# Kernel tuning notes

Hardware: AMD Instinct MI355X
Metric: run time of the kernel (lower is better)

## Reference

```python
import jax, jax.numpy as jnp
import numpy as np

N_NODES = 10000
N_EDGES = 60000
D = 128          # latent_size
L = 15           # num_layers
EPS = 1e-5       # LayerNorm eps (torch default)


def _layernorm(h, g, b):
    mu = jnp.mean(h, axis=-1, keepdims=True)
    var = jnp.mean(jnp.square(h - mu), axis=-1, keepdims=True)
    return (h - mu) * jax.lax.rsqrt(var + EPS) * g + b


def _mlp(h, w1, b1, g1, bt1, w2, b2, g2, bt2):
    # Linear -> LayerNorm -> GELU(exact) -> [Dropout: identity in eval] -> Linear -> LayerNorm
    h = _layernorm(h @ w1 + b1, g1, bt1)
    h = jax.nn.gelu(h, approximate=False)
    return _layernorm(h @ w2 + b2, g2, bt2)


def setup_inputs() -> dict:
    key = jax.random.key(0)
    ks = jax.random.split(key, 20)
    x = jax.random.normal(ks[0], (N_NODES, D), dtype=jnp.float32)
    edge_index = jax.random.randint(ks[1], (2, N_EDGES), 0, N_NODES, dtype=jnp.int32)
    edge_attr = jax.random.normal(ks[2], (N_EDGES, D), dtype=jnp.float32)
    s = 0.02
    # Edge MLP params: Linear(3D->2D), LN(2D), Linear(2D->D), LN(D), stacked over L layers
    ew1 = jax.random.normal(ks[3], (L, 3 * D, 2 * D), dtype=jnp.float32) * s
    eb1 = jnp.zeros((L, 2 * D), dtype=jnp.float32)
    eg1 = jnp.ones((L, 2 * D), dtype=jnp.float32)
    ebt1 = jnp.zeros((L, 2 * D), dtype=jnp.float32)
    ew2 = jax.random.normal(ks[4], (L, 2 * D, D), dtype=jnp.float32) * s
    eb2 = jnp.zeros((L, D), dtype=jnp.float32)
    eg2 = jnp.ones((L, D), dtype=jnp.float32)
    ebt2 = jnp.zeros((L, D), dtype=jnp.float32)
    # Node MLP params: Linear(2D->2D), LN(2D), Linear(2D->D), LN(D)
    nw1 = jax.random.normal(ks[5], (L, 2 * D, 2 * D), dtype=jnp.float32) * s
    nb1 = jnp.zeros((L, 2 * D), dtype=jnp.float32)
    ng1 = jnp.ones((L, 2 * D), dtype=jnp.float32)
    nbt1 = jnp.zeros((L, 2 * D), dtype=jnp.float32)
    nw2 = jax.random.normal(ks[6], (L, 2 * D, D), dtype=jnp.float32) * s
    nb2 = jnp.zeros((L, D), dtype=jnp.float32)
    ng2 = jnp.ones((L, D), dtype=jnp.float32)
    nbt2 = jnp.zeros((L, D), dtype=jnp.float32)
    return dict(x=x, edge_index=edge_index, edge_attr=edge_attr,
                ew1=ew1, eb1=eb1, eg1=eg1, ebt1=ebt1, ew2=ew2, eb2=eb2, eg2=eg2, ebt2=ebt2,
                nw1=nw1, nb1=nb1, ng1=ng1, nbt1=nbt1, nw2=nw2, nb2=nb2, ng2=ng2, nbt2=nbt2)


def reference(x, edge_index, edge_attr,
              ew1, eb1, eg1, ebt1, ew2, eb2, eg2, ebt2,
              nw1, nb1, ng1, nbt1, nw2, nb2, ng2, nbt2):
    row, col = edge_index[0], edge_index[1]
    # neighbor counts (per destination node), clamped to >= 1; constant across layers
    count = jax.ops.segment_sum(jnp.ones((edge_index.shape[1],), dtype=x.dtype), col,
                                num_segments=x.shape[0])
    count = jnp.maximum(count, 1.0)[:, None]  # [N,1]
    for i in range(L):
        edge_input = jnp.concatenate([x[row], x[col], edge_attr], axis=1)  # [E, 3D]
        edge_attr = edge_attr + _mlp(edge_input, ew1[i], eb1[i], eg1[i], ebt1[i],
                                     ew2[i], eb2[i], eg2[i], ebt2[i])
        agg = jax.ops.segment_sum(edge_attr, col, num_segments=x.shape[0]) / count  # [N, D]
        node_input = jnp.concatenate([x, agg], axis=1)  # [N, 2D]
        x = x + _mlp(node_input, nw1[i], nb1[i], ng1[i], nbt1[i],
                     nw2[i], nb2[i], ng2[i], nbt2[i])
    return x, edge_attr
```

## Files before the change

### kernel.cpp

```cpp
#include <hip/hip_runtime.h>
#include <hip/hip_bf16.h>
#include <math.h>

#define NN 10000
#define NE 60000
#define DD 128
#define NL 15
#define LN_EPS 1e-5f

typedef __attribute__((ext_vector_type(8))) short short8;
typedef __attribute__((ext_vector_type(4))) float floatx4;

__device__ __forceinline__ unsigned short f2bf(float f) {
    unsigned u = __float_as_uint(f);
    u += 0x7fff + ((u >> 16) & 1);
    return (unsigned short)(u >> 16);
}
__device__ __forceinline__ unsigned bc2(float a, float b) {
    __hip_bfloat162 t = __float22bfloat162_rn(make_float2(a, b));
    return *(unsigned*)&t;
}
__device__ __forceinline__ float bfl(unsigned w) { return __uint_as_float(w << 16); }
__device__ __forceinline__ float bfh(unsigned w) { return __uint_as_float(w & 0xffff0000u); }
__device__ __forceinline__ float gelu_fast(float y) {
    float u = y * y;
    float s2 = y * fmaf(u, 0.07135481283f, 1.59576912161f);
    return y * __builtin_amdgcn_rcpf(1.0f + __expf(-s2));
}

__device__ __forceinline__ void pack_one(const float* __restrict__ W, unsigned short* __restrict__ P,
                                         int u, int Kk, int Nk, bool perm) {
    int per_layer = Kk * Nk;
    int i = u / per_layer;
    int v0 = u - i * per_layer;
    int S = Kk >> 5;
    int t = v0 / (S * 512);
    int rem = v0 - t * (S * 512);
    int s = rem >> 9;
    int v = rem & 511;
    int l = v >> 3, j = v & 7;
    int kv = (s << 5) + ((l >> 4) << 3) + j;
    int k = perm ? (((kv & 15) << 4) | (kv >> 4)) : kv;
    int n = (t << 4) + (l & 15);
    P[u] = f2bf(W[((size_t)i * Kk + k) * Nk + n]);
}

#define N_EW1 (NL * 384 * 256)
#define N_EW2 (NL * 256 * 128)
#define N_NW1 (NL * 256 * 256)
#define N_NW2 (NL * 256 * 128)

__global__ void pack_all(const float* __restrict__ ew1, const float* __restrict__ ew2,
                         const float* __restrict__ nw1, const float* __restrict__ nw2,
                         unsigned short* __restrict__ P) {
    int tid = blockIdx.x * blockDim.x + threadIdx.x;
    if (tid < N_EW1) { pack_one(ew1, P, tid, 384, 256, false); return; }
    tid -= N_EW1;
    if (tid < N_EW2) { pack_one(ew2, P + N_EW1, tid, 256, 128, true); return; }
    tid -= N_EW2;
    if (tid < N_NW1) { pack_one(nw1, P + N_EW1 + N_EW2, tid, 256, 256, false); return; }
    tid -= N_NW1;
    if (tid < N_NW2) { pack_one(nw2, P + N_EW1 + N_EW2 + N_NW1, tid, 256, 128, true); return; }
}

__global__ void hist_kernel(const int* __restrict__ ecol, int* __restrict__ cnt) {
    int e = blockIdx.x * blockDim.x + threadIdx.x;
    if (e < NE) atomicAdd(&cnt[ecol[e]], 1);
}

__global__ void scan_kernel(const int* __restrict__ cnt, int* __restrict__ starts,
                            int* __restrict__ cursor, float* __restrict__ cinv) {
    __shared__ int part[256];
    int t = threadIdx.x;
    const int chunk = (NN + 255) / 256;
    int lo = t * chunk;
    int hi = lo + chunk; if (hi > NN) hi = NN;
    int s = 0;
    for (int n = lo; n < hi; ++n) s += cnt[n];
    part[t] = s;
    __syncthreads();
    for (int off = 1; off < 256; off <<= 1) {
        int v = (t >= off) ? part[t - off] : 0;
        __syncthreads();
        part[t] += v;
        __syncthreads();
    }
    int base = part[t] - s;
    for (int n = lo; n < hi; ++n) {
        int c = cnt[n];
        starts[n] = base; cursor[n] = base;
        cinv[n] = 1.0f / (float)(c > 0 ? c : 1);
        base += c;
    }
}

__global__ void fill_kernel(const int* __restrict__ ecol, int* __restrict__ cursor,
                            int* __restrict__ eidx) {
    int e = blockIdx.x * blockDim.x + threadIdx.x;
    if (e < NE) {
        int slot = atomicAdd(&cursor[ecol[e]], 1);
        eidx[slot] = e;
    }
}

__global__ void init_shadow(const float* __restrict__ x, const float* __restrict__ ea,
                            unsigned short* __restrict__ xb, unsigned short* __restrict__ eb) {
    int t = blockIdx.x * blockDim.x + threadIdx.x;
    const int NX = NN * DD / 4;
    const int NEA = NE * DD / 4;
    if (t < NX) {
        float4 v = *(const float4*)&x[(size_t)t * 4];
        uint2 p; p.x = bc2(v.x, v.y); p.y = bc2(v.z, v.w);
        *(uint2*)&xb[(size_t)t * 4] = p;
    } else if (t < NX + NEA) {
        size_t u = (size_t)(t - NX);
        float4 v = *(const float4*)&ea[u * 4];
        uint2 p; p.x = bc2(v.x, v.y); p.y = bc2(v.z, v.w);
        *(uint2*)&eb[u * 4] = p;
    }
}

template <int K1, int ROWS_TOTAL, int ROWS, bool EDGE>
__global__ __launch_bounds__(ROWS * 8, 4)
void mlp_mfma(const unsigned short* __restrict__ xb16,
              const int* __restrict__ erow, const int* __restrict__ ecol,
              const unsigned short* __restrict__ eas16,
              const int* __restrict__ starts, const int* __restrict__ cnt,
              const float* __restrict__ cinv, const int* __restrict__ eidx,
              float* __restrict__ target,
              unsigned short* __restrict__ shadow,
              const unsigned short* __restrict__ W1p, const unsigned short* __restrict__ W2p,
              const float* __restrict__ b1, const float* __restrict__ g1, const float* __restrict__ bt1,
              const float* __restrict__ b2, const float* __restrict__ g2, const float* __restrict__ bt2)
{
    constexpr int S1 = K1 / 32;
    __shared__ union {
        unsigned short a1[ROWS * K1];
        unsigned short h[ROWS * 256];
    } sm;
    __shared__ float red1[ROWS][8];
    __shared__ float red2[ROWS][8];

    const int tid  = threadIdx.x;
    const int lane = tid & 63;
    const int w    = tid >> 6;
    const int q    = lane >> 4;
    const int c15  = lane & 15;
    const int r0   = blockIdx.x * ROWS;

    const int qn = w & 3;
    const int pm = w >> 2;
    const int mp = w >> 2;
    const int np = w & 3;

    {
        const int r = tid >> 3;
        const int g = tid & 7;
        const int row_g = r0 + r;
        const bool ok = (ROWS_TOTAL % ROWS == 0) || (row_g < ROWS_TOTAL);
        const int rg = ok ? row_g : 0;
        if constexpr (EDGE) {
            const unsigned short* baseA = &xb16[(size_t)erow[rg] * DD];
            const unsigned short* baseB = &xb16[(size_t)ecol[rg] * DD];
            const unsigned short* baseC = &eas16[(size_t)rg * DD];
            #pragma unroll
            for (int it = 0; it < 6; ++it) {
                const int gg = g + 8 * it;
                const int p = gg << 3;
                const unsigned short* src = (p < 128) ? (baseA + p)
                                          : (p < 256) ? (baseB + (p - 128))
                                                      : (baseC + (p - 256));
                uint4 v = *(const uint4*)src;
                *(uint4*)&sm.a1[r * K1 + ((gg ^ (r & 7)) << 3)] = v;
            }
        } else {
            const unsigned short* baseA = &xb16[(size_t)rg * DD];
            #pragma unroll
            for (int it = 0; it < 2; ++it) {
                const int gg = g + 8 * it;
                uint4 v = *(const uint4*)(baseA + (gg << 3));
                *(uint4*)&sm.a1[r * K1 + ((gg ^ (r & 7)) << 3)] = v;
            }
            const int st = starts[rg];
            const int de = cnt[rg];
            const float ci = cinv[rg];
            float4 sa0 = {0.f,0.f,0.f,0.f}, sa1 = sa0, sb0 = sa0, sb1 = sa0;
            for (int i = 0; i < de; ++i) {
                const int e = eidx[st + i];
                const unsigned short* er = &eas16[(size_t)e * DD + (g << 3)];
                uint4 a = *(const uint4*)er;
                uint4 b = *(const uint4*)(er + 64);
                sa0.x += bfl(a.x); sa0.y += bfh(a.x); sa0.z += bfl(a.y); sa0.w += bfh(a.y);
                sa1.x += bfl(a.z); sa1.y += bfh(a.z); sa1.z += bfl(a.w); sa1.w += bfh(a.w);
                sb0.x += bfl(b.x); sb0.y += bfh(b.x); sb0.z += bfl(b.y); sb0.w += bfh(b.y);
                sb1.x += bfl(b.z); sb1.y += bfh(b.z); sb1.z += bfl(b.w); sb1.w += bfh(b.w);
            }
            uint4 v;
            v.x = bc2(sa0.x * ci, sa0.y * ci); v.y = bc2(sa0.z * ci, sa0.w * ci);
            v.z = bc2(sa1.x * ci, sa1.y * ci); v.w = bc2(sa1.z * ci, sa1.w * ci);
            const int gg2 = g + 16;
            *(uint4*)&sm.a1[r * K1 + ((gg2 ^ (r & 7)) << 3)] = v;
            v.x = bc2(sb0.x * ci, sb0.y * ci); v.y = bc2(sb0.z * ci, sb0.w * ci);
            v.z = bc2(sb1.x * ci, sb1.y * ci); v.w = bc2(sb1.z * ci, sb1.w * ci);
            const int gg3 = g + 24;
            *(uint4*)&sm.a1[r * K1 + ((gg3 ^ (r & 7)) << 3)] = v;
        }
    }
    __syncthreads();

    float b2c[2], g2c[2], t2c[2];
    #pragma unroll
    for (int jn = 0; jn < 2; ++jn) {
        int col = (((np << 1) + jn) << 4) + c15;
        b2c[jn] = b2[col]; g2c[jn] = g2[col]; t2c[jn] = bt2[col];
    }

    floatx4 acc[2][4];
    #pragma unroll
    for (int mt = 0; mt < 2; ++mt)
        #pragma unroll
        for (int ntl = 0; ntl < 4; ++ntl)
            acc[mt][ntl] = (floatx4){0.f, 0.f, 0.f, 0.f};

    __builtin_amdgcn_s_setprio(1);
    #pragma unroll
    for (int s = 0; s < S1; ++s) {
        short8 af[2];
        #pragma unroll
        for (int mt = 0; mt < 2; ++mt) {
            int row  = (((pm << 1) + mt) << 4) + c15;
            int kgrp = ((s << 2) + q) ^ (row & 7);
            af[mt] = *(const short8*)&sm.a1[row * K1 + (kgrp << 3)];
        }
        #pragma unroll
        for (int ntl = 0; ntl < 4; ++ntl) {
            const short8 bf = *(const short8*)&W1p[((((((qn << 2) + ntl) * S1) + s) << 6) + lane) << 3];
            #pragma unroll
            for (int mt = 0; mt < 2; ++mt)
                acc[mt][ntl] = __builtin_amdgcn_mfma_f32_16x16x32_bf16(af[mt], bf, acc[mt][ntl], 0, 0, 0);
        }
    }
    __builtin_amdgcn_s_setprio(0);

    float tpre[2][4][2];
    if constexpr (EDGE) {
        #pragma unroll
        for (int jm = 0; jm < 2; ++jm)
            #pragma unroll
            for (int r = 0; r < 4; ++r) {
                int row = (((mp << 1) + jm) << 4) + (q << 2) + r;
                #pragma unroll
                for (int jn = 0; jn < 2; ++jn) {
                    int col = (((np << 1) + jn) << 4) + c15;
                    int vc = 256 + col;
                    int addr = row * K1 + ((((vc >> 3) ^ (row & 7)) << 3) | (vc & 7));
                    tpre[jm][r][jn] = __uint_as_float((unsigned)sm.a1[addr] << 16);
                }
            }
    }

    float b1c[4], g1c[4], t1c[4];
    #pragma unroll
    for (int ntl = 0; ntl < 4; ++ntl) {
        int col = (((qn << 2) + ntl) << 4) + c15;
        b1c[ntl] = b1[col]; g1c[ntl] = g1[col]; t1c[ntl] = bt1[col];
    }
    #pragma unroll
    for (int mt = 0; mt < 2; ++mt)
        #pragma unroll
        for (int r = 0; r < 4; ++r) {
            float p = 0.f, sq = 0.f;
            #pragma unroll
            for (int ntl = 0; ntl < 4; ++ntl) {
                float v = acc[mt][ntl][r] + b1c[ntl];
                acc[mt][ntl][r] = v;
                p += v; sq += v * v;
            }
            p += __shfl_xor(p, 1);  sq += __shfl_xor(sq, 1);
            p += __shfl_xor(p, 2);  sq += __shfl_xor(sq, 2);
            p += __shfl_xor(p, 4);  sq += __shfl_xor(sq, 4);
            p += __shfl_xor(p, 8);  sq += __shfl_xor(sq, 8);
            if (c15 == 0) {
                int row = (((pm << 1) + mt) << 4) + (q << 2) + r;
                red1[row][(qn << 1) + 0] = p;
                red1[row][(qn << 1) + 1] = sq;
            }
        }
    __syncthreads();

    #pragma unroll
    for (int mt = 0; mt < 2; ++mt)
        #pragma unroll
        for (int r = 0; r < 4; ++r) {
            int row = (((pm << 1) + mt) << 4) + (q << 2) + r;
            const float4 p0 = *(const float4*)&red1[row][0];
            const float4 p1 = *(const float4*)&red1[row][4];
            float p  = p0.x + p0.z + p1.x + p1.z;
            float sq = p0.y + p0.w + p1.y + p1.w;
            float mu = p * (1.0f / 256.0f);
            float rs = rsqrtf(sq * (1.0f / 256.0f) - mu * mu + LN_EPS);
            float y0 = gelu_fast((acc[mt][0][r] - mu) * rs * g1c[0] + t1c[0]);
            float y1 = gelu_fast((acc[mt][1][r] - mu) * rs * g1c[1] + t1c[1]);
            float y2 = gelu_fast((acc[mt][2][r] - mu) * rs * g1c[2] + t1c[2]);
            float y3 = gelu_fast((acc[mt][3][r] - mu) * rs * g1c[3] + t1c[3]);
            uint2 hp;
            hp.x = bc2(y0, y1);
            hp.y = bc2(y2, y3);
            int gg = (c15 << 1) + (qn >> 1);
            int addr = row * 256 + (((gg ^ (row & 7)) << 3) | ((qn & 1) << 2));
            *(uint2*)&sm.h[addr] = hp;
        }
    __syncthreads();

    floatx4 acc2[2][2];
    #pragma unroll
    for (int jm = 0; jm < 2; ++jm)
        #pragma unroll
        for (int jn = 0; jn < 2; ++jn)
            acc2[jm][jn] = (floatx4){0.f, 0.f, 0.f, 0.f};

    __builtin_amdgcn_s_setprio(1);
    #pragma unroll
    for (int s = 0; s < 8; ++s) {
        short8 a2[2];
        #pragma unroll
        for (int jm = 0; jm < 2; ++jm) {
            int mrow = (((mp << 1) + jm) << 4) + c15;
            int kgrp = ((s << 2) + q) ^ (mrow & 7);
            a2[jm] = *(const short8*)&sm.h[mrow * 256 + (kgrp << 3)];
        }
        #pragma unroll
        for (int jn = 0; jn < 2; ++jn) {
            int nt = (np << 1) + jn;
            const short8 b = *(const short8*)&W2p[((((nt << 3) + s) << 6) + lane) << 3];
            #pragma unroll
            for (int jm = 0; jm < 2; ++jm)
                acc2[jm][jn] = __builtin_amdgcn_mfma_f32_16x16x32_bf16(a2[jm], b, acc2[jm][jn], 0, 0, 0);
        }
    }
    __builtin_amdgcn_s_setprio(0);

    if constexpr (!EDGE) {
        #pragma unroll
        for (int jm = 0; jm < 2; ++jm)
            #pragma unroll
            for (int r = 0; r < 4; ++r) {
                int row = (((mp << 1) + jm) << 4) + (q << 2) + r;
                int rowg = r0 + row;
                const bool okk = (ROWS_TOTAL % ROWS == 0) || (rowg < ROWS_TOTAL);
                const int rgs = okk ? rowg : 0;
                #pragma unroll
                for (int jn = 0; jn < 2; ++jn) {
                    int col = (((np << 1) + jn) << 4) + c15;
                    tpre[jm][r][jn] = target[(size_t)rgs * DD + col];
                }
            }
    }

    #pragma unroll
    for (int jm = 0; jm < 2; ++jm)
        #pragma unroll
        for (int r = 0; r < 4; ++r) {
            float p = 0.f, sq = 0.f;
            #pragma unroll
            for (int jn = 0; jn < 2; ++jn) {
                float v = acc2[jm][jn][r] + b2c[jn];
                acc2[jm][jn][r] = v;
                p += v; sq += v * v;
            }
            p += __shfl_xor(p, 1);  sq += __shfl_xor(sq, 1);
            p += __shfl_xor(p, 2);  sq += __shfl_xor(sq, 2);
            p += __shfl_xor(p, 4);  sq += __shfl_xor(sq, 4);
            p += __shfl_xor(p, 8);  sq += __shfl_xor(sq, 8);
            if (c15 == 0) {
                int row = (((mp << 1) + jm) << 4) + (q << 2) + r;
                red2[row][(np << 1) + 0] = p;
                red2[row][(np << 1) + 1] = sq;
            }
        }
    __syncthreads();

    #pragma unroll
    for (int jm = 0; jm < 2; ++jm)
        #pragma unroll
        for (int r = 0; r < 4; ++r) {
            int row = (((mp << 1) + jm) << 4) + (q << 2) + r;
            const float4 pp0 = *(const float4*)&red2[row][0];
            const float4 pp1 = *(const float4*)&red2[row][4];
            float p  = pp0.x + pp0.z + pp1.x + pp1.z;
            float sq = pp0.y + pp0.w + pp1.y + pp1.w;
            float mu = p * (1.0f / 128.0f);
            float rs = rsqrtf(sq * (1.0f / 128.0f) - mu * mu + LN_EPS);
            int rowg = r0 + row;
            if (ROWS_TOTAL % ROWS == 0 || rowg < ROWS_TOTAL) {
                #pragma unroll
                for (int jn = 0; jn < 2; ++jn) {
                    int col = (((np << 1) + jn) << 4) + c15;
                    float o = (acc2[jm][jn][r] - mu) * rs * g2c[jn] + t2c[jn];
                    float t = tpre[jm][r][jn] + o;
                    shadow[(size_t)rowg * DD + col] = f2bf(t);
                    if constexpr (EDGE) {
                        if (target) target[(size_t)rowg * DD + col] = t;
                    } else {
                        target[(size_t)rowg * DD + col] = t;
                    }
                }
            }
        }
}

extern "C" void kernel_launch(void* const* d_in, const int* in_sizes, int n_in,
                              void* d_out, int out_size, void* d_ws, size_t ws_size,
                              hipStream_t stream) {
    const float* x_in  = (const float*)d_in[0];
    const int*   ei    = (const int*)  d_in[1];
    const float* ea_in = (const float*)d_in[2];
    const float* ew1 = (const float*)d_in[3];
    const float* eb1 = (const float*)d_in[4];
    const float* eg1 = (const float*)d_in[5];
    const float* ebt1= (const float*)d_in[6];
    const float* ew2 = (const float*)d_in[7];
    const float* eb2 = (const float*)d_in[8];
    const float* eg2 = (const float*)d_in[9];
    const float* ebt2= (const float*)d_in[10];
    const float* nw1 = (const float*)d_in[11];
    const float* nb1 = (const float*)d_in[12];
    const float* ng1 = (const float*)d_in[13];
    const float* nbt1= (const float*)d_in[14];
    const float* nw2 = (const float*)d_in[15];
    const float* nb2 = (const float*)d_in[16];
    const float* ng2 = (const float*)d_in[17];
    const float* nbt2= (const float*)d_in[18];

    const int* erow = ei;
    const int* ecol = ei + NE;

    float* xbuf  = (float*)d_out;
    float* eabuf = (float*)d_out + NN * DD;

    unsigned short* ew1p  = (unsigned short*)d_ws;
    unsigned short* ew2p  = ew1p + N_EW1;
    unsigned short* nw1p  = ew2p + N_EW2;
    unsigned short* nw2p  = nw1p + N_NW1;
    unsigned short* xb16  = nw2p + N_NW2;
    unsigned short* eas16 = xb16 + (size_t)NN * DD;
    int*   cnt    = (int*)(eas16 + (size_t)NE * DD);
    int*   starts = cnt + NN;
    int*   cursor = starts + NN;
    int*   eidx   = cursor + NN;
    float* cinv   = (float*)(eidx + NE);

    hipMemcpyAsync(xbuf, x_in, (size_t)NN * DD * sizeof(float), hipMemcpyDeviceToDevice, stream);

    hipMemsetAsync(cnt, 0, NN * sizeof(int), stream);
    hist_kernel<<<(NE + 255) / 256, 256, 0, stream>>>(ecol, cnt);
    scan_kernel<<<1, 256, 0, stream>>>(cnt, starts, cursor, cinv);
    fill_kernel<<<(NE + 255) / 256, 256, 0, stream>>>(ecol, cursor, eidx);

    {
        int ntot = (NN * DD + NE * DD) / 4;
        init_shadow<<<(ntot + 255) / 256, 256, 0, stream>>>(x_in, ea_in, xb16, eas16);
    }

    {
        int ntot = N_EW1 + N_EW2 + N_NW1 + N_NW2;
        pack_all<<<(ntot + 255) / 256, 256, 0, stream>>>(ew1, ew2, nw1, nw2, ew1p);
    }

    for (int i = 0; i < NL; ++i) {
        mlp_mfma<384, NE, 32, true><<<NE / 32, 256, 0, stream>>>(
            xb16, erow, ecol, eas16, nullptr, nullptr, nullptr, nullptr,
            (i == NL - 1) ? eabuf : nullptr, eas16,
            ew1p + (size_t)i * 384 * 256, ew2p + (size_t)i * 256 * 128,
            eb1 + (size_t)i * 256, eg1 + (size_t)i * 256, ebt1 + (size_t)i * 256,
            eb2 + (size_t)i * 128, eg2 + (size_t)i * 128, ebt2 + (size_t)i * 128);
        mlp_mfma<256, NN, 32, false><<<(NN + 31) / 32, 256, 0, stream>>>(
            xb16, nullptr, nullptr, eas16, starts, cnt, cinv, eidx,
            xbuf, xb16,
            nw1p + (size_t)i * 256 * 256, nw2p + (size_t)i * 256 * 128,
            nb1 + (size_t)i * 256, ng1 + (size_t)i * 256, nbt1 + (size_t)i * 256,
            nb2 + (size_t)i * 128, ng2 + (size_t)i * 128, nbt2 + (size_t)i * 128);
    }
}
```

Measured before the change: 1.137 ms.

## Double edge MLP tile to 64 rows and stage bf16 shadow stores through LDS

The edge MLP kernel now processes 64 edges per block instead of 32. Every wave covers all row tiles, so each weight fragment loaded from global memory feeds more MFMAs. This halves the weight re-reads across blocks. The bf16 edge shadow output is first written to shared memory and then copied out as coalesced 16-byte row stores, replacing scattered 2-byte stores. In exchange, accumulator register pressure rises, shared memory per block doubles and the launch-bounds occupancy target drops, which may reduce latency hiding.

```diff
diff --git a/kernel.cpp b/kernel.cpp
--- a/kernel.cpp
+++ b/kernel.cpp
@@ -121,7 +121,7 @@
 }
 
 template <int K1, int ROWS_TOTAL, int ROWS, bool EDGE>
-__global__ __launch_bounds__(ROWS * 8, 4)
+__global__ __launch_bounds__(256, 128 / ROWS)
 void mlp_mfma(const unsigned short* __restrict__ xb16,
               const int* __restrict__ erow, const int* __restrict__ ecol,
               const unsigned short* __restrict__ eas16,
@@ -134,6 +134,7 @@
               const float* __restrict__ b2, const float* __restrict__ g2, const float* __restrict__ bt2)
 {
     constexpr int S1 = K1 / 32;
+    constexpr int MT = ROWS / 16;
     __shared__ union {
         unsigned short a1[ROWS * K1];
         unsigned short h[ROWS * 256];
@@ -149,62 +150,63 @@
     const int r0   = blockIdx.x * ROWS;
 
     const int qn = w & 3;
-    const int pm = w >> 2;
-    const int mp = w >> 2;
     const int np = w & 3;
 
-    {
+    if constexpr (EDGE) {
+        const int r = tid >> 2;
+        const int g = tid & 3;
+        const int row_g = r0 + r;
+        const bool ok = (ROWS_TOTAL % ROWS == 0) || (row_g < ROWS_TOTAL);
+        const int rg = ok ? row_g : 0;
+        const unsigned short* baseA = &xb16[(size_t)erow[rg] * DD];
+        const unsigned short* baseB = &xb16[(size_t)ecol[rg] * DD];
+        const unsigned short* baseC = &eas16[(size_t)rg * DD];
+        #pragma unroll
+        for (int it = 0; it < 12; ++it) {
+            const int gg = g + 4 * it;
+            const int p = gg << 3;
+            const unsigned short* src = (p < 128) ? (baseA + p)
+                                      : (p < 256) ? (baseB + (p - 128))
+                                                  : (baseC + (p - 256));
+            uint4 v = *(const uint4*)src;
+            *(uint4*)&sm.a1[r * K1 + ((gg ^ (r & 7)) << 3)] = v;
+        }
+    } else {
         const int r = tid >> 3;
         const int g = tid & 7;
         const int row_g = r0 + r;
         const bool ok = (ROWS_TOTAL % ROWS == 0) || (row_g < ROWS_TOTAL);
         const int rg = ok ? row_g : 0;
-        if constexpr (EDGE) {
-            const unsigned short* baseA = &xb16[(size_t)erow[rg] * DD];
-            const unsigned short* baseB = &xb16[(size_t)ecol[rg] * DD];
-            const unsigned short* baseC = &eas16[(size_t)rg * DD];
-            #pragma unroll
-            for (int it = 0; it < 6; ++it) {
-                const int gg = g + 8 * it;
-                const int p = gg << 3;
-                const unsigned short* src = (p < 128) ? (baseA + p)
-                                          : (p < 256) ? (baseB + (p - 128))
-                                                      : (baseC + (p - 256));
-                uint4 v = *(const uint4*)src;
-                *(uint4*)&sm.a1[r * K1 + ((gg ^ (r & 7)) << 3)] = v;
-            }
-        } else {
-            const unsigned short* baseA = &xb16[(size_t)rg * DD];
-            #pragma unroll
-            for (int it = 0; it < 2; ++it) {
-                const int gg = g + 8 * it;
-                uint4 v = *(const uint4*)(baseA + (gg << 3));
-                *(uint4*)&sm.a1[r * K1 + ((gg ^ (r & 7)) << 3)] = v;
-            }
-            const int st = starts[rg];
-            const int de = cnt[rg];
-            const float ci = cinv[rg];
-            float4 sa0 = {0.f,0.f,0.f,0.f}, sa1 = sa0, sb0 = sa0, sb1 = sa0;
-            for (int i = 0; i < de; ++i) {
-                const int e = eidx[st + i];
-                const unsigned short* er = &eas16[(size_t)e * DD + (g << 3)];
-                uint4 a = *(const uint4*)er;
-                uint4 b = *(const uint4*)(er + 64);
-                sa0.x += bfl(a.x); sa0.y += bfh(a.x); sa0.z += bfl(a.y); sa0.w += bfh(a.y);
-                sa1.x += bfl(a.z); sa1.y += bfh(a.z); sa1.z += bfl(a.w); sa1.w += bfh(a.w);
-                sb0.x += bfl(b.x); sb0.y += bfh(b.x); sb0.z += bfl(b.y); sb0.w += bfh(b.y);
-                sb1.x += bfl(b.z); sb1.y += bfh(b.z); sb1.z += bfl(b.w); sb1.w += bfh(b.w);
-            }
-            uint4 v;
-            v.x = bc2(sa0.x * ci, sa0.y * ci); v.y = bc2(sa0.z * ci, sa0.w * ci);
-            v.z = bc2(sa1.x * ci, sa1.y * ci); v.w = bc2(sa1.z * ci, sa1.w * ci);
-            const int gg2 = g + 16;
-            *(uint4*)&sm.a1[r * K1 + ((gg2 ^ (r & 7)) << 3)] = v;
-            v.x = bc2(sb0.x * ci, sb0.y * ci); v.y = bc2(sb0.z * ci, sb0.w * ci);
-            v.z = bc2(sb1.x * ci, sb1.y * ci); v.w = bc2(sb1.z * ci, sb1.w * ci);
-            const int gg3 = g + 24;
-            *(uint4*)&sm.a1[r * K1 + ((gg3 ^ (r & 7)) << 3)] = v;
-        }
+        const unsigned short* baseA = &xb16[(size_t)rg * DD];
+        #pragma unroll
+        for (int it = 0; it < 2; ++it) {
+            const int gg = g + 8 * it;
+            uint4 v = *(const uint4*)(baseA + (gg << 3));
+            *(uint4*)&sm.a1[r * K1 + ((gg ^ (r & 7)) << 3)] = v;
+        }
+        const int st = starts[rg];
+        const int de = cnt[rg];
+        const float ci = cinv[rg];
+        float4 sa0 = {0.f,0.f,0.f,0.f}, sa1 = sa0, sb0 = sa0, sb1 = sa0;
+        for (int i = 0; i < de; ++i) {
+            const int e = eidx[st + i];
+            const unsigned short* er = &eas16[(size_t)e * DD + (g << 3)];
+            uint4 a = *(const uint4*)er;
+            uint4 b = *(const uint4*)(er + 64);
+            sa0.x += bfl(a.x); sa0.y += bfh(a.x); sa0.z += bfl(a.y); sa0.w += bfh(a.y);
+            sa1.x += bfl(a.z); sa1.y += bfh(a.z); sa1.z += bfl(a.w); sa1.w += bfh(a.w);
+            sb0.x += bfl(b.x); sb0.y += bfh(b.x); sb0.z += bfl(b.y); sb0.w += bfh(b.y);
+            sb1.x += bfl(b.z); sb1.y += bfh(b.z); sb1.z += bfl(b.w); sb1.w += bfh(b.w);
+        }
+        uint4 v;
+        v.x = bc2(sa0.x * ci, sa0.y * ci); v.y = bc2(sa0.z * ci, sa0.w * ci);
+        v.z = bc2(sa1.x * ci, sa1.y * ci); v.w = bc2(sa1.z * ci, sa1.w * ci);
+        const int gg2 = g + 16;
+        *(uint4*)&sm.a1[r * K1 + ((gg2 ^ (r & 7)) << 3)] = v;
+        v.x = bc2(sb0.x * ci, sb0.y * ci); v.y = bc2(sb0.z * ci, sb0.w * ci);
+        v.z = bc2(sb1.x * ci, sb1.y * ci); v.w = bc2(sb1.z * ci, sb1.w * ci);
+        const int gg3 = g + 24;
+        *(uint4*)&sm.a1[r * K1 + ((gg3 ^ (r & 7)) << 3)] = v;
     }
     __syncthreads();
 
@@ -215,9 +217,9 @@
         b2c[jn] = b2[col]; g2c[jn] = g2[col]; t2c[jn] = bt2[col];
     }
 
-    floatx4 acc[2][4];
-    #pragma unroll
-    for (int mt = 0; mt < 2; ++mt)
+    floatx4 acc[MT][4];
+    #pragma unroll
+    for (int mt = 0; mt < MT; ++mt)
         #pragma unroll
         for (int ntl = 0; ntl < 4; ++ntl)
             acc[mt][ntl] = (floatx4){0.f, 0.f, 0.f, 0.f};
@@ -225,10 +227,10 @@
     __builtin_amdgcn_s_setprio(1);
     #pragma unroll
     for (int s = 0; s < S1; ++s) {
-        short8 af[2];
-        #pragma unroll
-        for (int mt = 0; mt < 2; ++mt) {
-            int row  = (((pm << 1) + mt) << 4) + c15;
+        short8 af[MT];
+        #pragma unroll
+        for (int mt = 0; mt < MT; ++mt) {
+            int row  = (mt << 4) + c15;
             int kgrp = ((s << 2) + q) ^ (row & 7);
             af[mt] = *(const short8*)&sm.a1[row * K1 + (kgrp << 3)];
         }
@@ -236,19 +238,19 @@
         for (int ntl = 0; ntl < 4; ++ntl) {
             const short8 bf = *(const short8*)&W1p[((((((qn << 2) + ntl) * S1) + s) << 6) + lane) << 3];
             #pragma unroll
-            for (int mt = 0; mt < 2; ++mt)
+            for (int mt = 0; mt < MT; ++mt)
                 acc[mt][ntl] = __builtin_amdgcn_mfma_f32_16x16x32_bf16(af[mt], bf, acc[mt][ntl], 0, 0, 0);
         }
     }
     __builtin_amdgcn_s_setprio(0);
 
-    float tpre[2][4][2];
+    float tpre[MT][4][2];
     if constexpr (EDGE) {
         #pragma unroll
-        for (int jm = 0; jm < 2; ++jm)
+        for (int jm = 0; jm < MT; ++jm)
             #pragma unroll
             for (int r = 0; r < 4; ++r) {
-                int row = (((mp << 1) + jm) << 4) + (q << 2) + r;
+                int row = (jm << 4) + (q << 2) + r;
                 #pragma unroll
                 for (int jn = 0; jn < 2; ++jn) {
                     int col = (((np << 1) + jn) << 4) + c15;
@@ -266,7 +268,7 @@
         b1c[ntl] = b1[col]; g1c[ntl] = g1[col]; t1c[ntl] = bt1[col];
     }
     #pragma unroll
-    for (int mt = 0; mt < 2; ++mt)
+    for (int mt = 0; mt < MT; ++mt)
         #pragma unroll
         for (int r = 0; r < 4; ++r) {
             float p = 0.f, sq = 0.f;
@@ -281,7 +283,7 @@
             p += __shfl_xor(p, 4);  sq += __shfl_xor(sq, 4);
             p += __shfl_xor(p, 8);  sq += __shfl_xor(sq, 8);
             if (c15 == 0) {
-                int row = (((pm << 1) + mt) << 4) + (q << 2) + r;
+                int row = (mt << 4) + (q << 2) + r;
                 red1[row][(qn << 1) + 0] = p;
                 red1[row][(qn << 1) + 1] = sq;
             }
@@ -289,10 +291,10 @@
     __syncthreads();
 
     #pragma unroll
-    for (int mt = 0; mt < 2; ++mt)
+    for (int mt = 0; mt < MT; ++mt)
         #pragma unroll
         for (int r = 0; r < 4; ++r) {
-            int row = (((pm << 1) + mt) << 4) + (q << 2) + r;
+            int row = (mt << 4) + (q << 2) + r;
             const float4 p0 = *(const float4*)&red1[row][0];
             const float4 p1 = *(const float4*)&red1[row][4];
             float p  = p0.x + p0.z + p1.x + p1.z;
@@ -312,9 +314,9 @@
         }
     __syncthreads();
 
-    floatx4 acc2[2][2];
-    #pragma unroll
-    for (int jm = 0; jm < 2; ++jm)
+    floatx4 acc2[MT][2];
+    #pragma unroll
+    for (int jm = 0; jm < MT; ++jm)
         #pragma unroll
         for (int jn = 0; jn < 2; ++jn)
             acc2[jm][jn] = (floatx4){0.f, 0.f, 0.f, 0.f};
@@ -322,10 +324,10 @@
     __builtin_amdgcn_s_setprio(1);
     #pragma unroll
     for (int s = 0; s < 8; ++s) {
-        short8 a2[2];
-        #pragma unroll
-        for (int jm = 0; jm < 2; ++jm) {
-            int mrow = (((mp << 1) + jm) << 4) + c15;
+        short8 a2[MT];
+        #pragma unroll
+        for (int jm = 0; jm < MT; ++jm) {
+            int mrow = (jm << 4) + c15;
             int kgrp = ((s << 2) + q) ^ (mrow & 7);
             a2[jm] = *(const short8*)&sm.h[mrow * 256 + (kgrp << 3)];
         }
@@ -334,7 +336,7 @@
             int nt = (np << 1) + jn;
             const short8 b = *(const short8*)&W2p[((((nt << 3) + s) << 6) + lane) << 3];
             #pragma unroll
-            for (int jm = 0; jm < 2; ++jm)
+            for (int jm = 0; jm < MT; ++jm)
                 acc2[jm][jn] = __builtin_amdgcn_mfma_f32_16x16x32_bf16(a2[jm], b, acc2[jm][jn], 0, 0, 0);
         }
     }
@@ -342,10 +344,10 @@
 
     if constexpr (!EDGE) {
         #pragma unroll
-        for (int jm = 0; jm < 2; ++jm)
+        for (int jm = 0; jm < MT; ++jm)
             #pragma unroll
             for (int r = 0; r < 4; ++r) {
-                int row = (((mp << 1) + jm) << 4) + (q << 2) + r;
+                int row = (jm << 4) + (q << 2) + r;
                 int rowg = r0 + row;
                 const bool okk = (ROWS_TOTAL % ROWS == 0) || (rowg < ROWS_TOTAL);
                 const int rgs = okk ? rowg : 0;
@@ -358,7 +360,7 @@
     }
 
     #pragma unroll
-    for (int jm = 0; jm < 2; ++jm)
+    for (int jm = 0; jm < MT; ++jm)
         #pragma unroll
         for (int r = 0; r < 4; ++r) {
             float p = 0.f, sq = 0.f;
@@ -373,7 +375,7 @@
             p += __shfl_xor(p, 4);  sq += __shfl_xor(sq, 4);
             p += __shfl_xor(p, 8);  sq += __shfl_xor(sq, 8);
             if (c15 == 0) {
-                int row = (((mp << 1) + jm) << 4) + (q << 2) + r;
+                int row = (jm << 4) + (q << 2) + r;
                 red2[row][(np << 1) + 0] = p;
                 red2[row][(np << 1) + 1] = sq;
             }
@@ -381,10 +383,10 @@
     __syncthreads();
 
     #pragma unroll
-    for (int jm = 0; jm < 2; ++jm)
+    for (int jm = 0; jm < MT; ++jm)
         #pragma unroll
         for (int r = 0; r < 4; ++r) {
-            int row = (((mp << 1) + jm) << 4) + (q << 2) + r;
+            int row = (jm << 4) + (q << 2) + r;
             const float4 pp0 = *(const float4*)&red2[row][0];
             const float4 pp1 = *(const float4*)&red2[row][4];
             float p  = pp0.x + pp0.z + pp1.x + pp1.z;
@@ -392,21 +394,39 @@
             float mu = p * (1.0f / 128.0f);
             float rs = rsqrtf(sq * (1.0f / 128.0f) - mu * mu + LN_EPS);
             int rowg = r0 + row;
-            if (ROWS_TOTAL % ROWS == 0 || rowg < ROWS_TOTAL) {
-                #pragma unroll
-                for (int jn = 0; jn < 2; ++jn) {
-                    int col = (((np << 1) + jn) << 4) + c15;
-                    float o = (acc2[jm][jn][r] - mu) * rs * g2c[jn] + t2c[jn];
-                    float t = tpre[jm][r][jn] + o;
-                    shadow[(size_t)rowg * DD + col] = f2bf(t);
-                    if constexpr (EDGE) {
-                        if (target) target[(size_t)rowg * DD + col] = t;
-                    } else {
+            const bool okk = (ROWS_TOTAL % ROWS == 0) || (rowg < ROWS_TOTAL);
+            #pragma unroll
+            for (int jn = 0; jn < 2; ++jn) {
+                int col = (((np << 1) + jn) << 4) + c15;
+                float o = (acc2[jm][jn][r] - mu) * rs * g2c[jn] + t2c[jn];
+                float t = tpre[jm][r][jn] + o;
+                if constexpr (EDGE) {
+                    int oaddr = row * 128 + ((((col >> 3) ^ (row & 7)) << 3) | (col & 7));
+                    sm.h[oaddr] = f2bf(t);
+                    if (target && okk) target[(size_t)rowg * DD + col] = t;
+                } else {
+                    if (okk) {
                         target[(size_t)rowg * DD + col] = t;
+                        shadow[(size_t)rowg * DD + col] = f2bf(t);
                     }
                 }
             }
         }
+
+    if constexpr (EDGE) {
+        __syncthreads();
+        const int rr = tid >> 2;
+        const int gq = tid & 3;
+        const int rg2 = r0 + rr;
+        if ((ROWS_TOTAL % ROWS == 0) || (rg2 < ROWS_TOTAL)) {
+            #pragma unroll
+            for (int k = 0; k < 4; ++k) {
+                int G = (gq << 2) + k;
+                uint4 v = *(const uint4*)&sm.h[rr * 128 + ((G ^ (rr & 7)) << 3)];
+                *(uint4*)&shadow[(size_t)rg2 * DD + (G << 3)] = v;
+            }
+        }
+    }
 }
 
 extern "C" void kernel_launch(void* const* d_in, const int* in_sizes, int n_in,
@@ -468,7 +488,7 @@
     }
 
     for (int i = 0; i < NL; ++i) {
-        mlp_mfma<384, NE, 32, true><<<NE / 32, 256, 0, stream>>>(
+        mlp_mfma<384, NE, 64, true><<<(NE + 63) / 64, 256, 0, stream>>>(
             xb16, erow, ecol, eas16, nullptr, nullptr, nullptr, nullptr,
             (i == NL - 1) ? eabuf : nullptr, eas16,
             ew1p + (size_t)i * 384 * 256, ew2p + (size_t)i * 256 * 128,
```

Measured after the change: 1.284 ms. 13.0% more time.

## Store edge features in destination-sorted order and stage edge output via LDS

Applied to the files above, without the earlier changes.

Edge data is permuted once into CSR (destination-sorted) order, so the node aggregation reads contiguous edge rows instead of gathering through eidx. Sorted row and column index arrays feed the edge kernel, and the final fp32 edge output is scattered back to the original order through eidx. The edge kernel's bf16 shadow output is staged in swizzled shared memory and written with coalesced 16-byte stores. This adds an extra syncthreads and a scattered final write, and the source-node gathers in the edge kernel lose some locality.

```diff
diff --git a/kernel.cpp b/kernel.cpp
--- a/kernel.cpp
+++ b/kernel.cpp
@@ -94,16 +94,21 @@
     }
 }
 
-__global__ void fill_kernel(const int* __restrict__ ecol, int* __restrict__ cursor,
-                            int* __restrict__ eidx) {
+__global__ void fill_kernel(const int* __restrict__ erow, const int* __restrict__ ecol,
+                            int* __restrict__ cursor, int* __restrict__ eidx,
+                            int* __restrict__ erow_s, int* __restrict__ ecol_s) {
     int e = blockIdx.x * blockDim.x + threadIdx.x;
     if (e < NE) {
-        int slot = atomicAdd(&cursor[ecol[e]], 1);
+        int c = ecol[e];
+        int slot = atomicAdd(&cursor[c], 1);
         eidx[slot] = e;
+        erow_s[slot] = erow[e];
+        ecol_s[slot] = c;
     }
 }
 
 __global__ void init_shadow(const float* __restrict__ x, const float* __restrict__ ea,
+                            const int* __restrict__ eidx,
                             unsigned short* __restrict__ xb, unsigned short* __restrict__ eb) {
     int t = blockIdx.x * blockDim.x + threadIdx.x;
     const int NX = NN * DD / 4;
@@ -114,19 +119,23 @@
         *(uint2*)&xb[(size_t)t * 4] = p;
     } else if (t < NX + NEA) {
         size_t u = (size_t)(t - NX);
-        float4 v = *(const float4*)&ea[u * 4];
+        int slot = (int)(u >> 5);
+        int j = (int)(u & 31);
+        int e = eidx[slot];
+        float4 v = *(const float4*)&ea[(size_t)e * DD + j * 4];
         uint2 p; p.x = bc2(v.x, v.y); p.y = bc2(v.z, v.w);
         *(uint2*)&eb[u * 4] = p;
     }
 }
 
-template <int K1, int ROWS_TOTAL, int ROWS, bool EDGE>
-__global__ __launch_bounds__(ROWS * 8, 4)
+template <int K1, int ROWS_TOTAL, bool EDGE>
+__global__ __launch_bounds__(256, 4)
 void mlp_mfma(const unsigned short* __restrict__ xb16,
               const int* __restrict__ erow, const int* __restrict__ ecol,
               const unsigned short* __restrict__ eas16,
               const int* __restrict__ starts, const int* __restrict__ cnt,
-              const float* __restrict__ cinv, const int* __restrict__ eidx,
+              const float* __restrict__ cinv,
+              const int* __restrict__ eidx,
               float* __restrict__ target,
               unsigned short* __restrict__ shadow,
               const unsigned short* __restrict__ W1p, const unsigned short* __restrict__ W2p,
@@ -134,6 +143,7 @@
               const float* __restrict__ b2, const float* __restrict__ g2, const float* __restrict__ bt2)
 {
     constexpr int S1 = K1 / 32;
+    constexpr int ROWS = 32;
     __shared__ union {
         unsigned short a1[ROWS * K1];
         unsigned short h[ROWS * 256];
@@ -149,8 +159,6 @@
     const int r0   = blockIdx.x * ROWS;
 
     const int qn = w & 3;
-    const int pm = w >> 2;
-    const int mp = w >> 2;
     const int np = w & 3;
 
     {
@@ -185,9 +193,8 @@
             const int de = cnt[rg];
             const float ci = cinv[rg];
             float4 sa0 = {0.f,0.f,0.f,0.f}, sa1 = sa0, sb0 = sa0, sb1 = sa0;
-            for (int i = 0; i < de; ++i) {
-                const int e = eidx[st + i];
-                const unsigned short* er = &eas16[(size_t)e * DD + (g << 3)];
+            const unsigned short* er = &eas16[(size_t)st * DD + (g << 3)];
+            for (int i = 0; i < de; ++i, er += DD) {
                 uint4 a = *(const uint4*)er;
                 uint4 b = *(const uint4*)(er + 64);
                 sa0.x += bfl(a.x); sa0.y += bfh(a.x); sa0.z += bfl(a.y); sa0.w += bfh(a.y);
@@ -228,7 +235,7 @@
         short8 af[2];
         #pragma unroll
         for (int mt = 0; mt < 2; ++mt) {
-            int row  = (((pm << 1) + mt) << 4) + c15;
+            int row  = (mt << 4) + c15;
             int kgrp = ((s << 2) + q) ^ (row & 7);
             af[mt] = *(const short8*)&sm.a1[row * K1 + (kgrp << 3)];
         }
@@ -248,7 +255,7 @@
         for (int jm = 0; jm < 2; ++jm)
             #pragma unroll
             for (int r = 0; r < 4; ++r) {
-                int row = (((mp << 1) + jm) << 4) + (q << 2) + r;
+                int row = (jm << 4) + (q << 2) + r;
                 #pragma unroll
                 for (int jn = 0; jn < 2; ++jn) {
                     int col = (((np << 1) + jn) << 4) + c15;
@@ -281,7 +288,7 @@
             p += __shfl_xor(p, 4);  sq += __shfl_xor(sq, 4);
             p += __shfl_xor(p, 8);  sq += __shfl_xor(sq, 8);
             if (c15 == 0) {
-                int row = (((pm << 1) + mt) << 4) + (q << 2) + r;
+                int row = (mt << 4) + (q << 2) + r;
                 red1[row][(qn << 1) + 0] = p;
                 red1[row][(qn << 1) + 1] = sq;
             }
@@ -292,7 +299,7 @@
     for (int mt = 0; mt < 2; ++mt)
         #pragma unroll
         for (int r = 0; r < 4; ++r) {
-            int row = (((pm << 1) + mt) << 4) + (q << 2) + r;
+            int row = (mt << 4) + (q << 2) + r;
             const float4 p0 = *(const float4*)&red1[row][0];
             const float4 p1 = *(const float4*)&red1[row][4];
             float p  = p0.x + p0.z + p1.x + p1.z;
@@ -325,7 +332,7 @@
         short8 a2[2];
         #pragma unroll
         for (int jm = 0; jm < 2; ++jm) {
-            int mrow = (((mp << 1) + jm) << 4) + c15;
+            int mrow = (jm << 4) + c15;
             int kgrp = ((s << 2) + q) ^ (mrow & 7);
             a2[jm] = *(const short8*)&sm.h[mrow * 256 + (kgrp << 3)];
         }
@@ -345,7 +352,7 @@
         for (int jm = 0; jm < 2; ++jm)
             #pragma unroll
             for (int r = 0; r < 4; ++r) {
-                int row = (((mp << 1) + jm) << 4) + (q << 2) + r;
+                int row = (jm << 4) + (q << 2) + r;
                 int rowg = r0 + row;
                 const bool okk = (ROWS_TOTAL % ROWS == 0) || (rowg < ROWS_TOTAL);
                 const int rgs = okk ? rowg : 0;
@@ -373,7 +380,7 @@
             p += __shfl_xor(p, 4);  sq += __shfl_xor(sq, 4);
             p += __shfl_xor(p, 8);  sq += __shfl_xor(sq, 8);
             if (c15 == 0) {
-                int row = (((mp << 1) + jm) << 4) + (q << 2) + r;
+                int row = (jm << 4) + (q << 2) + r;
                 red2[row][(np << 1) + 0] = p;
                 red2[row][(np << 1) + 1] = sq;
             }
@@ -384,7 +391,7 @@
     for (int jm = 0; jm < 2; ++jm)
         #pragma unroll
         for (int r = 0; r < 4; ++r) {
-            int row = (((mp << 1) + jm) << 4) + (q << 2) + r;
+            int row = (jm << 4) + (q << 2) + r;
             const float4 pp0 = *(const float4*)&red2[row][0];
             const float4 pp1 = *(const float4*)&red2[row][4];
             float p  = pp0.x + pp0.z + pp1.x + pp1.z;
@@ -392,21 +399,39 @@
             float mu = p * (1.0f / 128.0f);
             float rs = rsqrtf(sq * (1.0f / 128.0f) - mu * mu + LN_EPS);
             int rowg = r0 + row;
-            if (ROWS_TOTAL % ROWS == 0 || rowg < ROWS_TOTAL) {
-                #pragma unroll
-                for (int jn = 0; jn < 2; ++jn) {
-                    int col = (((np << 1) + jn) << 4) + c15;
-                    float o = (acc2[jm][jn][r] - mu) * rs * g2c[jn] + t2c[jn];
-                    float t = tpre[jm][r][jn] + o;
-                    shadow[(size_t)rowg * DD + col] = f2bf(t);
-                    if constexpr (EDGE) {
-                        if (target) target[(size_t)rowg * DD + col] = t;
-                    } else {
+            const bool okk = (ROWS_TOTAL % ROWS == 0) || (rowg < ROWS_TOTAL);
+            #pragma unroll
+            for (int jn = 0; jn < 2; ++jn) {
+                int col = (((np << 1) + jn) << 4) + c15;
+                float o = (acc2[jm][jn][r] - mu) * rs * g2c[jn] + t2c[jn];
+                float t = tpre[jm][r][jn] + o;
+                if constexpr (EDGE) {
+                    int oaddr = row * 128 + ((((col >> 3) ^ (row & 7)) << 3) | (col & 7));
+                    sm.h[oaddr] = f2bf(t);
+                    if (target) {
+                        int orig = eidx[rowg];
+                        target[(size_t)orig * DD + col] = t;
+                    }
+                } else {
+                    if (okk) {
                         target[(size_t)rowg * DD + col] = t;
+                        shadow[(size_t)rowg * DD + col] = f2bf(t);
                     }
                 }
             }
         }
+
+    if constexpr (EDGE) {
+        __syncthreads();
+        #pragma unroll
+        for (int k = 0; k < 2; ++k) {
+            int c = tid + (k << 8);
+            int row = c >> 4;
+            int G = c & 15;
+            uint4 v = *(const uint4*)&sm.h[row * 128 + ((G ^ (row & 7)) << 3)];
+            *(uint4*)&shadow[(size_t)(r0 + row) * DD + (G << 3)] = v;
+        }
+    }
 }
 
 extern "C" void kernel_launch(void* const* d_in, const int* in_sizes, int n_in,
@@ -448,18 +473,20 @@
     int*   starts = cnt + NN;
     int*   cursor = starts + NN;
     int*   eidx   = cursor + NN;
-    float* cinv   = (float*)(eidx + NE);
+    int*   erow_s = eidx + NE;
+    int*   ecol_s = erow_s + NE;
+    float* cinv   = (float*)(ecol_s + NE);
 
     hipMemcpyAsync(xbuf, x_in, (size_t)NN * DD * sizeof(float), hipMemcpyDeviceToDevice, stream);
 
     hipMemsetAsync(cnt, 0, NN * sizeof(int), stream);
     hist_kernel<<<(NE + 255) / 256, 256, 0, stream>>>(ecol, cnt);
     scan_kernel<<<1, 256, 0, stream>>>(cnt, starts, cursor, cinv);
-    fill_kernel<<<(NE + 255) / 256, 256, 0, stream>>>(ecol, cursor, eidx);
+    fill_kernel<<<(NE + 255) / 256, 256, 0, stream>>>(erow, ecol, cursor, eidx, erow_s, ecol_s);
 
     {
         int ntot = (NN * DD + NE * DD) / 4;
-        init_shadow<<<(ntot + 255) / 256, 256, 0, stream>>>(x_in, ea_in, xb16, eas16);
+        init_shadow<<<(ntot + 255) / 256, 256, 0, stream>>>(x_in, ea_in, eidx, xb16, eas16);
     }
 
     {
@@ -468,14 +495,14 @@
     }
 
     for (int i = 0; i < NL; ++i) {
-        mlp_mfma<384, NE, 32, true><<<NE / 32, 256, 0, stream>>>(
-            xb16, erow, ecol, eas16, nullptr, nullptr, nullptr, nullptr,
+        mlp_mfma<384, NE, true><<<NE / 32, 256, 0, stream>>>(
+            xb16, erow_s, ecol_s, eas16, nullptr, nullptr, nullptr, eidx,
             (i == NL - 1) ? eabuf : nullptr, eas16,
             ew1p + (size_t)i * 384 * 256, ew2p + (size_t)i * 256 * 128,
             eb1 + (size_t)i * 256, eg1 + (size_t)i * 256, ebt1 + (size_t)i * 256,
             eb2 + (size_t)i * 128, eg2 + (size_t)i * 128, ebt2 + (size_t)i * 128);
-        mlp_mfma<256, NN, 32, false><<<(NN + 31) / 32, 256, 0, stream>>>(
-            xb16, nullptr, nullptr, eas16, starts, cnt, cinv, eidx,
+        mlp_mfma<256, NN, false><<<(NN + 31) / 32, 256, 0, stream>>>(
+            xb16, nullptr, nullptr, eas16, starts, cnt, cinv, nullptr,
             xbuf, xb16,
             nw1p + (size_t)i * 256 * 256, nw2p + (size_t)i * 256 * 128,
             nb1 + (size_t)i * 256, ng1 + (size_t)i * 256, nbt1 + (size_t)i * 256,
```

Result: faster. 1.104 ms (-2.9%).
